# Optimization experiments

Hardware: AMD Instinct MI355X
Metric: run time of the kernel (lower is better)

The kernel has to match this reference:

```python
import jax, jax.numpy as jnp
import numpy as np

B, NB, BS, C, H = 4, 128, 128, 256, 8  # batch, num_blocks, block_size, dim, heads


def setup_inputs() -> dict:
    key = jax.random.key(0)
    ks = jax.random.split(key, 8)
    x = jax.random.normal(ks[0], (B, NB * BS, C), dtype=jnp.float32)
    attn_mask = jax.random.randint(ks[1], (NB, BS, BS + 1), 0, 2, dtype=jnp.int32)
    # guarantee the global-node column is always attendable (avoids all--inf rows)
    attn_mask = attn_mask.at[:, :, BS].set(1)
    edge_feats = jax.random.normal(ks[2], (NB, BS, BS + 1, 4), dtype=jnp.float32)
    w_qkv = jax.random.normal(ks[3], (C, 3 * C), dtype=jnp.float32) * (C ** -0.5)
    b_qkv = jnp.zeros((3 * C,), dtype=jnp.float32)
    w_proj = jax.random.normal(ks[4], (C, C), dtype=jnp.float32) * (C ** -0.5)
    b_proj = jnp.zeros((C,), dtype=jnp.float32)
    w_gate = jax.random.normal(ks[5], (4, H), dtype=jnp.float32) * 0.01  # nn.init.normal_(std=0.01)
    b_gate = jnp.zeros((H,), dtype=jnp.float32)
    return {"x": x, "attn_mask": attn_mask, "edge_feats": edge_feats,
            "w_qkv": w_qkv, "b_qkv": b_qkv, "w_proj": w_proj, "b_proj": b_proj,
            "w_gate": w_gate, "b_gate": b_gate}


def reference(x, attn_mask, edge_feats, w_qkv, b_qkv, w_proj, b_proj, w_gate, b_gate):
    Bv, N, Cv = x.shape
    nb, bs, _ = attn_mask.shape
    Hv = b_gate.shape[0]
    hd = Cv // Hv
    scale = hd ** -0.5

    x_blk = x.reshape(Bv, nb, bs, Cv)
    block_node = x_blk.mean(axis=2, keepdims=True)           # [B, nb, 1, C]
    kv = jnp.concatenate([x_blk, block_node], axis=2)        # [B, nb, bs+1, C]

    qkv_q = x_blk @ w_qkv + b_qkv
    qkv_kv = kv @ w_qkv + b_qkv
    q = qkv_q[..., :Cv].reshape(Bv, nb, bs, Hv, hd)
    k = qkv_kv[..., Cv:2 * Cv].reshape(Bv, nb, bs + 1, Hv, hd)
    v = qkv_kv[..., 2 * Cv:].reshape(Bv, nb, bs + 1, Hv, hd)

    scores = jnp.einsum('bnqhd,bnkhd->bnqkh', q, k) * scale  # [B, nb, bs, bs+1, H]

    # physics bias: zero out (with channel-3 = 1) at the global-node column and the diagonal
    qi = jnp.arange(bs)[:, None]
    ki = jnp.arange(bs + 1)[None, :]
    special = (ki == bs) | (ki == qi)                        # [bs, bs+1]
    special_vec = jnp.array([0.0, 0.0, 0.0, 1.0], dtype=x.dtype)
    bias = jnp.where(special[:, :, None], special_vec, edge_feats[..., :4])  # [nb, bs, bs+1, 4]
    bias = jnp.broadcast_to(bias[None], (Bv, nb, bs, bs + 1, 4))

    scores = scores + bias[..., 3:4]
    mask = (attn_mask[None, :, :, :, None] != 0)             # [1, nb, bs, bs+1, 1]
    scores = jnp.where(mask, scores, -jnp.inf)
    probs = jax.nn.softmax(scores, axis=3)

    gate = jnp.where(mask, bias @ w_gate + b_gate, jnp.zeros((), dtype=x.dtype))
    combined = probs + gate                                  # [B, nb, bs, bs+1, H]

    out = jnp.einsum('bnqkh,bnkhd->bnqhd', combined, v).reshape(Bv, N, Cv)
    return out @ w_proj + b_proj
```

## Files before the change

### kernel.cpp

```cpp
#include <hip/hip_runtime.h>

#define B_   4
#define NB_  128
#define BS_  128
#define C_   256
#define H_   8
#define KL_  129
#define SC2_   0.25503486f
#define LOG2E_ 1.4426950408889634f
#define LN2_   0.6931471805599453f
#define RSTR_  99072

typedef unsigned short u16;
typedef unsigned int   u32;
typedef short          s16;
typedef __attribute__((ext_vector_type(8))) __bf16 bf16x8;
typedef __attribute__((ext_vector_type(4))) float  f32x4;

__device__ __forceinline__ float bf16tof(u16 u) {
  union { u32 i; float f; } v; v.i = ((u32)u) << 16; return v.f;
}
__device__ __forceinline__ u16 fbits(float a) {
  union { __bf16 h; u16 u; } v; v.h = (__bf16)a; return v.u;
}
__device__ __forceinline__ u32 pk2(float a, float b) {
  union { __bf16 h[2]; u32 u; } v;
  v.h[0] = (__bf16)a; v.h[1] = (__bf16)b;
  return v.u;
}
__device__ __forceinline__ float asf(u32 u) {
  union { u32 i; float f; } v; v.i = u; return v.f;
}

__device__ __forceinline__ void glds16(const void* g, void* l) {
  __builtin_amdgcn_global_load_lds(
      (const __attribute__((address_space(1))) unsigned int*)g,
      (__attribute__((address_space(3))) unsigned int*)l, 16, 0, 0);
}

__global__ __launch_bounds__(256) void meancvt_kernel(const float* __restrict__ x,
                                                      u16* __restrict__ xb) {
  const int blk = blockIdx.x;
  const int c = threadIdx.x;
  const float* p = x + (size_t)blk * BS_ * C_ + c;
  u16* q = xb + (size_t)blk * (KL_ * C_) + c;
  float s = 0.f;
  #pragma unroll 4
  for (int r = 0; r < BS_; ++r) {
    const float v = p[(size_t)r * C_];
    s += v;
    q[(size_t)r * C_] = fbits(v);
  }
  q[(size_t)BS_ * C_] = fbits(s * (1.0f / BS_));
}

__global__ __launch_bounds__(256) void wt_kernel(const float* __restrict__ wq,
      const float* __restrict__ wp, s16* __restrict__ wtq, s16* __restrict__ wtp) {
  const int i = blockIdx.x * 256 + threadIdx.x;
  if (i < 768 * 256) {
    const int nn = i >> 8, k = i & 255;
    wtq[i] = (s16)fbits(wq[k * 768 + nn]);
  } else {
    const int j = i - 768 * 256;
    const int nn = j >> 8, k = j & 255;
    wtp[j] = (s16)fbits(wp[k * 256 + nn]);
  }
}

__global__ __launch_bounds__(256) void pre_kernel(const int* __restrict__ mask,
      const float* __restrict__ ef, u16* __restrict__ e4t) {
  const int t = blockIdx.x * 256 + threadIdx.x;
  const int kq = t & 31;
  const int row = t >> 5;
  const int q = row & 127;
  const int key0 = kq * 4;
  const int* mrow = mask + (size_t)row * KL_;
  const float* erow = ef + (size_t)row * KL_ * 4;
  u32 o[8];
  #pragma unroll
  for (int r = 0; r < 4; ++r) {
    const int key = key0 + r;
    const int m = mrow[key];
    float4 e = *(const float4*)(erow + (size_t)key * 4);
    if (key == q) { e.x = 0.f; e.y = 0.f; e.z = 0.f; e.w = 1.f; }
    float e3L = e.w * LOG2E_;
    if (!m) { e.x = 0.f; e.y = 0.f; e.z = 0.f; e3L = -1e30f; }
    o[2*r]   = pk2(e.x, e.y);
    o[2*r+1] = pk2(e.z, e3L);
  }
  uint4* dst = (uint4*)(e4t + (size_t)row * 512 + key0 * 4);
  dst[0] = uint4{o[0], o[1], o[2], o[3]};
  dst[1] = uint4{o[4], o[5], o[6], o[7]};
}

template<bool STRIDED, bool OBF16, int NS>
__global__ __launch_bounds__(256) void mfma_gemm(const s16* __restrict__ Ab,
      const s16* __restrict__ Bt, const float* __restrict__ bias,
      void* __restrict__ outv) {
  __shared__ __align__(16) s16 Al[2][128 * 64];
  __shared__ __align__(16) s16 Bl[2][128 * 64];
  const int tid = threadIdx.x;
  const int lane = tid & 63;
  const int wid = tid >> 6;
  constexpr int ncol = NS / 128;
  const int per  = gridDim.x >> 3;
  const int gidx = (blockIdx.x & 7) * per + (blockIdx.x >> 3);
  const int arow = gidx / ncol;
  const int col0 = (gidx - arow * ncol) * 128;
  const int row0 = arow * 128;
  const int ldrow = lane >> 3;
  const int lcb   = (lane & 7) * 16;

  auto STAGE = [&](int k0, int buf) {
    #pragma unroll
    for (int j = 0; j < 4; ++j) {
      const int c = wid * 4 + j;
      const int row = c * 8 + ldrow;
      const int scb = lcb ^ ((row & 7) << 4);
      glds16(Bt + (size_t)(col0 + row) * C_ + k0 + (scb >> 1), &Bl[buf][c * 512]);
    }
    #pragma unroll
    for (int j = 0; j < 4; ++j) {
      const int c = wid * 4 + j;
      const int row = c * 8 + ldrow;
      const int scb = lcb ^ ((row & 7) << 4);
      if constexpr (STRIDED)
        glds16(Ab + (size_t)arow * RSTR_ + (size_t)row * 768 + 256
                  + k0 + (scb >> 1), &Al[buf][c * 512]);
      else
        glds16(Ab + (size_t)(row0 + row) * C_ + k0 + (scb >> 1), &Al[buf][c * 512]);
    }
  };

  f32x4 acc[4][4];
  #pragma unroll
  for (int i = 0; i < 4; ++i)
    #pragma unroll
    for (int j = 0; j < 4; ++j) acc[i][j] = f32x4{0.f, 0.f, 0.f, 0.f};

  STAGE(0, 0);
  __syncthreads();

  const int fr = lane & 15;
  const int ar0 = (wid >> 1) * 64;
  const int ac0 = (wid & 1) * 64;
  #pragma unroll 1
  for (int t = 0; t < 4; ++t) {
    if (t < 3) STAGE((t + 1) * 64, (t + 1) & 1);
    const char* Ac = (const char*)&Al[t & 1][0];
    const char* Bc = (const char*)&Bl[t & 1][0];
    #pragma unroll
    for (int kk = 0; kk < 64; kk += 32) {
      const int kb = kk * 2 + (lane >> 4) * 16;
      bf16x8 af[4], bfr[4];
      #pragma unroll
      for (int mf = 0; mf < 4; ++mf) {
        const int row = ar0 + mf * 16 + fr;
        af[mf] = *(const bf16x8*)(Ac + row * 128 + (kb ^ ((row & 7) << 4)));
      }
      #pragma unroll
      for (int nf = 0; nf < 4; ++nf) {
        const int row = ac0 + nf * 16 + fr;
        bfr[nf] = *(const bf16x8*)(Bc + row * 128 + (kb ^ ((row & 7) << 4)));
      }
      #pragma unroll
      for (int mf = 0; mf < 4; ++mf)
        #pragma unroll
        for (int nf = 0; nf < 4; ++nf)
          acc[mf][nf] = __builtin_amdgcn_mfma_f32_16x16x32_bf16(
              af[mf], bfr[nf], acc[mf][nf], 0, 0, 0);
    }
    __syncthreads();
  }

  const int orow0 = row0 + (wid >> 1) * 64 + (lane >> 4) * 4;
  const int ocol0 = col0 + (wid & 1) * 64 + (lane & 15);
  #pragma unroll
  for (int nf = 0; nf < 4; ++nf) {
    const int col = ocol0 + nf * 16;
    const float bb = bias[col];
    #pragma unroll
    for (int mf = 0; mf < 4; ++mf) {
      #pragma unroll
      for (int r = 0; r < 4; ++r) {
        const size_t row = (size_t)(orow0 + mf * 16 + r);
        const float v = acc[mf][nf][r] + bb;
        if constexpr (OBF16) ((u16*)outv)[row * NS + col] = fbits(v);
        else                 ((float*)outv)[row * NS + col] = v;
      }
    }
  }
}

__global__ __launch_bounds__(256, 4) void attn_kernel(u16* __restrict__ qkv,
      const u16* __restrict__ e4t, const float* __restrict__ wg_,
      const float* __restrict__ bg) {
  __shared__ __align__(16) char lds[36176];
  const int bid = blockIdx.x;
  const int xcd = bid & 7;
  const int j   = bid >> 3;
  const int wgi = xcd * 64 + (j >> 3);
  const int h   = j & 7;
  const int n = wgi & (NB_ - 1);
  const int tid = threadIdx.x;
  const int wid = tid >> 6, lane = tid & 63;
  const int g = lane >> 4, ql = lane & 15;
  u16*  Kl = (u16*)lds;
  u16*  vt = (u16*)(lds + 10320);
  char* pb = lds + 18768 + wid * 4352;

  u16* qkv_blk = qkv + (size_t)wgi * RSTR_;
  const u16* ebase = e4t + (size_t)n * (128 * 512);

  for (int i = tid; i < 516; i += 256) {
    const int r = i >> 2, dc = i & 3;
    const uint4 u = *(const uint4*)(qkv_blk + (size_t)r * 768 + 256 + h * 32 + dc * 8);
    *(uint4*)(Kl + r * 40 + dc * 8) = u;
  }
  for (int i = tid; i < 512; i += 256) {
    const int r = i >> 2, dc = i & 3;
    const uint4 u = *(const uint4*)(qkv_blk + (size_t)r * 768 + 512 + h * 32 + dc * 8);
    u16* col = vt + (dc * 8) * 132 + r;
    col[0 * 132] = (u16)(u.x & 0xffff); col[1 * 132] = (u16)(u.x >> 16);
    col[2 * 132] = (u16)(u.y & 0xffff); col[3 * 132] = (u16)(u.y >> 16);
    col[4 * 132] = (u16)(u.z & 0xffff); col[5 * 132] = (u16)(u.z >> 16);
    col[6 * 132] = (u16)(u.w & 0xffff); col[7 * 132] = (u16)(u.w >> 16);
  }
  __syncthreads();

  const float v128a = bf16tof(qkv_blk[(size_t)128 * 768 + 512 + h * 32 + ql]);
  const float v128b = bf16tof(qkv_blk[(size_t)128 * 768 + 512 + h * 32 + 16 + ql]);

  const float wgc0 = wg_[h], wgc1 = wg_[8 + h], wgc2 = wg_[16 + h];
  const float wgc3s = wg_[24 + h] * LN2_;
  const float bgh = bg[h];
  const float gk128 = wg_[24 + h] + bgh;

  #pragma unroll 1
  for (int mi = 0; mi < 2; ++mi) {
    const int mt = wid * 2 + mi;
    const int qrow = mt * 16 + ql;
    const bf16x8 qf = *(const bf16x8*)(qkv_blk + (size_t)qrow * 768 + h * 32 + g * 8);
    const uint4* eql = (const uint4*)(ebase + (size_t)qrow * 512) + 2 * g;

    float psum = 0.f;
    uint2 gab[8];
    #pragma unroll
    for (int f = 0; f < 8; ++f) {
      const bf16x8 kf = *(const bf16x8*)(Kl + (16 * f + ql) * 40 + 8 * g);
      f32x4 st = __builtin_amdgcn_mfma_f32_16x16x32_bf16(
          kf, qf, f32x4{0.f, 0.f, 0.f, 0.f}, 0, 0, 0);
      const uint4 ea = eql[8 * f];
      const uint4 eb = eql[8 * f + 1];
      const u32 wa[4] = {ea.x, ea.z, eb.x, eb.z};
      const u32 wb[4] = {ea.y, ea.w, eb.y, eb.w};
      float w[4], gt[4];
      #pragma unroll
      for (int r = 0; r < 4; ++r) {
        const float e0 = asf(wa[r] << 16), e1 = asf(wa[r] & 0xffff0000u);
        const float e2 = asf(wb[r] << 16), e3L = asf(wb[r] & 0xffff0000u);
        const float gg = fmaf(e0, wgc0, fmaf(e1, wgc1,
                          fmaf(e2, wgc2, fmaf(e3L, wgc3s, bgh))));
        gt[r] = (e3L > -1e29f) ? gg : 0.f;
        w[r] = __builtin_amdgcn_exp2f(fmaf(st[r], SC2_, e3L));
        psum += w[r];
      }
      gab[f] = uint2{pk2(gt[0], gt[1]), pk2(gt[2], gt[3])};
      *(uint2*)(pb + ql * 272 + (16 * f + 4 * g) * 2) =
          uint2{pk2(w[0], w[1]), pk2(w[2], w[3])};
    }
    const bf16x8 kf8 = *(const bf16x8*)(Kl + 128 * 40 + 8 * g);
    f32x4 st8 = __builtin_amdgcn_mfma_f32_16x16x32_bf16(
        kf8, qf, f32x4{0.f, 0.f, 0.f, 0.f}, 0, 0, 0);
    const float w0 = __builtin_amdgcn_exp2f(
        fmaf(st8[0], SC2_, (g == 0) ? LOG2E_ : -1e30f));
    psum += w0;
    psum += __shfl_xor(psum, 16);
    psum += __shfl_xor(psum, 32);
    const float inv = __builtin_amdgcn_rcpf(psum);
    const float c128 = fmaf(w0, inv, (g == 0) ? gk128 : 0.f);

    f32x4 ow0{0.f,0.f,0.f,0.f}, ow1{0.f,0.f,0.f,0.f};
    #pragma unroll
    for (int c = 0; c < 4; ++c) {
      const bf16x8 pa = *(const bf16x8*)(pb + ql * 272 + (32 * c + 8 * g) * 2);
      const bf16x8 v0 = *(const bf16x8*)(vt + ql * 132 + 32 * c + 8 * g);
      const bf16x8 v1 = *(const bf16x8*)(vt + (16 + ql) * 132 + 32 * c + 8 * g);
      ow0 = __builtin_amdgcn_mfma_f32_16x16x32_bf16(pa, v0, ow0, 0, 0, 0);
      ow1 = __builtin_amdgcn_mfma_f32_16x16x32_bf16(pa, v1, ow1, 0, 0, 0);
    }
    #pragma unroll
    for (int f = 0; f < 8; ++f)
      *(uint2*)(pb + ql * 272 + (16 * f + 4 * g) * 2) = gab[f];
    f32x4 og0{0.f,0.f,0.f,0.f}, og1{0.f,0.f,0.f,0.f};
    #pragma unroll
    for (int c = 0; c < 4; ++c) {
      const bf16x8 pa = *(const bf16x8*)(pb + ql * 272 + (32 * c + 8 * g) * 2);
      const bf16x8 v0 = *(const bf16x8*)(vt + ql * 132 + 32 * c + 8 * g);
      const bf16x8 v1 = *(const bf16x8*)(vt + (16 + ql) * 132 + 32 * c + 8 * g);
      og0 = __builtin_amdgcn_mfma_f32_16x16x32_bf16(pa, v0, og0, 0, 0, 0);
      og1 = __builtin_amdgcn_mfma_f32_16x16x32_bf16(pa, v1, og1, 0, 0, 0);
    }
    u16* aop = qkv_blk + (size_t)(mt * 16 + g * 4) * 768 + 256 + h * 32 + ql;
    #pragma unroll
    for (int r = 0; r < 4; ++r) {
      const float iv = __shfl(inv,  4 * g + r);
      const float cc = __shfl(c128, 4 * g + r);
      aop[(size_t)r * 768]      = fbits(fmaf(cc, v128a, fmaf(ow0[r], iv, og0[r])));
      aop[(size_t)r * 768 + 16] = fbits(fmaf(cc, v128b, fmaf(ow1[r], iv, og1[r])));
    }
  }
}

extern "C" void kernel_launch(void* const* d_in, const int* in_sizes, int n_in,
                              void* d_out, int out_size, void* d_ws, size_t ws_size,
                              hipStream_t stream) {
  (void)in_sizes; (void)n_in; (void)out_size; (void)ws_size;
  const float* x      = (const float*)d_in[0];
  const int*   mask   = (const int*)  d_in[1];
  const float* ef     = (const float*)d_in[2];
  const float* w_qkv  = (const float*)d_in[3];
  const float* b_qkv  = (const float*)d_in[4];
  const float* w_proj = (const float*)d_in[5];
  const float* b_proj = (const float*)d_in[6];
  const float* w_gate = (const float*)d_in[7];
  const float* b_gate = (const float*)d_in[8];
  float* out = (float*)d_out;
  char* ws = (char*)d_ws;

  u16* qkv = (u16*)(ws);
  s16* wtq = (s16*)(ws + 101449728);
  s16* wtp = (s16*)(ws + 101842944);
  u16* xb  = (u16*)(ws + 101974016);
  u16* e4t = (u16*)(ws + 101974016);

  meancvt_kernel<<<B_ * NB_, 256, 0, stream>>>(x, xb);
  wt_kernel<<<(768 * 256 + 256 * 256) / 256, 256, 0, stream>>>(
      w_qkv, w_proj, wtq, wtp);
  mfma_gemm<false, true, 768>
      <<<(B_ * NB_ * KL_ / 128) * 6, 256, 0, stream>>>(
      (const s16*)xb, wtq, b_qkv, qkv);
  pre_kernel<<<(NB_ * BS_ * 32) / 256, 256, 0, stream>>>(mask, ef, e4t);
  attn_kernel<<<B_ * NB_ * H_, 256, 0, stream>>>(
      qkv, (const u16*)e4t, w_gate, b_gate);
  mfma_gemm<true, false, 256>
      <<<(B_ * NB_ * BS_ / 128) * 2, 256, 0, stream>>>(
      (const s16*)qkv, wtp, b_proj, out);
}
```

Measured before the change: 196.8 us.

## Precompute per-head gate tables and a separate score-bias table in pre_kernel

Result: faster. 190.9 us, median of 2 (-3.0%).

```diff
diff --git a/kernel.cpp b/kernel.cpp
--- a/kernel.cpp
+++ b/kernel.cpp
@@ -8,7 +8,6 @@
 #define KL_  129
 #define SC2_   0.25503486f
 #define LOG2E_ 1.4426950408889634f
-#define LN2_   0.6931471805599453f
 #define RSTR_  99072
 
 typedef unsigned short u16;
@@ -68,29 +67,46 @@
 }
 
 __global__ __launch_bounds__(256) void pre_kernel(const int* __restrict__ mask,
-      const float* __restrict__ ef, u16* __restrict__ e4t) {
+      const float* __restrict__ ef, const float* __restrict__ wg_,
+      const float* __restrict__ bg, u16* __restrict__ g4t,
+      u16* __restrict__ s4t) {
   const int t = blockIdx.x * 256 + threadIdx.x;
   const int kq = t & 31;
   const int row = t >> 5;
+  const int n = row >> 7;
   const int q = row & 127;
   const int key0 = kq * 4;
   const int* mrow = mask + (size_t)row * KL_;
   const float* erow = ef + (size_t)row * KL_ * 4;
-  u32 o[8];
+  float e0[4], e1[4], e2[4], e3[4];
+  int m[4];
   #pragma unroll
   for (int r = 0; r < 4; ++r) {
     const int key = key0 + r;
-    const int m = mrow[key];
-    float4 e = *(const float4*)(erow + (size_t)key * 4);
-    if (key == q) { e.x = 0.f; e.y = 0.f; e.z = 0.f; e.w = 1.f; }
-    float e3L = e.w * LOG2E_;
-    if (!m) { e.x = 0.f; e.y = 0.f; e.z = 0.f; e3L = -1e30f; }
-    o[2*r]   = pk2(e.x, e.y);
-    o[2*r+1] = pk2(e.z, e3L);
-  }
-  uint4* dst = (uint4*)(e4t + (size_t)row * 512 + key0 * 4);
-  dst[0] = uint4{o[0], o[1], o[2], o[3]};
-  dst[1] = uint4{o[4], o[5], o[6], o[7]};
+    m[r] = mrow[key];
+    float4 ev = *(const float4*)(erow + (size_t)key * 4);
+    if (key == q) { ev.x = 0.f; ev.y = 0.f; ev.z = 0.f; ev.w = 1.f; }
+    e0[r] = ev.x; e1[r] = ev.y; e2[r] = ev.z; e3[r] = ev.w;
+  }
+  float s[4];
+  #pragma unroll
+  for (int r = 0; r < 4; ++r) s[r] = m[r] ? e3[r] * LOG2E_ : -1e30f;
+  *(uint2*)(s4t + (size_t)row * 128 + key0) =
+      uint2{pk2(s[0], s[1]), pk2(s[2], s[3])};
+  #pragma unroll
+  for (int h = 0; h < 8; ++h) {
+    const float w0 = wg_[h], w1 = wg_[8 + h], w2 = wg_[16 + h],
+                w3 = wg_[24 + h], bh = bg[h];
+    float gt[4];
+    #pragma unroll
+    for (int r = 0; r < 4; ++r) {
+      const float gg = fmaf(e0[r], w0, fmaf(e1[r], w1,
+                        fmaf(e2[r], w2, fmaf(e3[r], w3, bh))));
+      gt[r] = m[r] ? gg : 0.f;
+    }
+    *(uint2*)(g4t + (((size_t)n * 8 + h) * 128 + q) * 128 + key0) =
+        uint2{pk2(gt[0], gt[1]), pk2(gt[2], gt[3])};
+  }
 }
 
 template<bool STRIDED, bool OBF16, int NS>
@@ -193,8 +209,8 @@
 }
 
 __global__ __launch_bounds__(256, 4) void attn_kernel(u16* __restrict__ qkv,
-      const u16* __restrict__ e4t, const float* __restrict__ wg_,
-      const float* __restrict__ bg) {
+      const u16* __restrict__ g4t, const u16* __restrict__ s4t,
+      const float* __restrict__ wg_, const float* __restrict__ bg) {
   __shared__ __align__(16) char lds[36176];
   const int bid = blockIdx.x;
   const int xcd = bid & 7;
@@ -210,7 +226,8 @@
   char* pb = lds + 18768 + wid * 4352;
 
   u16* qkv_blk = qkv + (size_t)wgi * RSTR_;
-  const u16* ebase = e4t + (size_t)n * (128 * 512);
+  const u16* sbase = s4t + (size_t)n * (128 * 128);
+  const u16* gbase = g4t + ((size_t)n * 8 + h) * (128 * 128);
 
   for (int i = tid; i < 516; i += 256) {
     const int r = i >> 2, dc = i & 3;
@@ -230,18 +247,15 @@
 
   const float v128a = bf16tof(qkv_blk[(size_t)128 * 768 + 512 + h * 32 + ql]);
   const float v128b = bf16tof(qkv_blk[(size_t)128 * 768 + 512 + h * 32 + 16 + ql]);
-
-  const float wgc0 = wg_[h], wgc1 = wg_[8 + h], wgc2 = wg_[16 + h];
-  const float wgc3s = wg_[24 + h] * LN2_;
-  const float bgh = bg[h];
-  const float gk128 = wg_[24 + h] + bgh;
+  const float gk128 = wg_[24 + h] + bg[h];
 
   #pragma unroll 1
   for (int mi = 0; mi < 2; ++mi) {
     const int mt = wid * 2 + mi;
     const int qrow = mt * 16 + ql;
     const bf16x8 qf = *(const bf16x8*)(qkv_blk + (size_t)qrow * 768 + h * 32 + g * 8);
-    const uint4* eql = (const uint4*)(ebase + (size_t)qrow * 512) + 2 * g;
+    const u16* srow = sbase + (size_t)qrow * 128;
+    const u16* grow = gbase + (size_t)qrow * 128;
 
     float psum = 0.f;
     uint2 gab[8];
@@ -250,22 +264,14 @@
       const bf16x8 kf = *(const bf16x8*)(Kl + (16 * f + ql) * 40 + 8 * g);
       f32x4 st = __builtin_amdgcn_mfma_f32_16x16x32_bf16(
           kf, qf, f32x4{0.f, 0.f, 0.f, 0.f}, 0, 0, 0);
-      const uint4 ea = eql[8 * f];
-      const uint4 eb = eql[8 * f + 1];
-      const u32 wa[4] = {ea.x, ea.z, eb.x, eb.z};
-      const u32 wb[4] = {ea.y, ea.w, eb.y, eb.w};
-      float w[4], gt[4];
-      #pragma unroll
-      for (int r = 0; r < 4; ++r) {
-        const float e0 = asf(wa[r] << 16), e1 = asf(wa[r] & 0xffff0000u);
-        const float e2 = asf(wb[r] << 16), e3L = asf(wb[r] & 0xffff0000u);
-        const float gg = fmaf(e0, wgc0, fmaf(e1, wgc1,
-                          fmaf(e2, wgc2, fmaf(e3L, wgc3s, bgh))));
-        gt[r] = (e3L > -1e29f) ? gg : 0.f;
-        w[r] = __builtin_amdgcn_exp2f(fmaf(st[r], SC2_, e3L));
-        psum += w[r];
-      }
-      gab[f] = uint2{pk2(gt[0], gt[1]), pk2(gt[2], gt[3])};
+      const uint2 sv = *(const uint2*)(srow + 16 * f + 4 * g);
+      gab[f] = *(const uint2*)(grow + 16 * f + 4 * g);
+      float w[4];
+      w[0] = __builtin_amdgcn_exp2f(fmaf(st[0], SC2_, asf(sv.x << 16)));
+      w[1] = __builtin_amdgcn_exp2f(fmaf(st[1], SC2_, asf(sv.x & 0xffff0000u)));
+      w[2] = __builtin_amdgcn_exp2f(fmaf(st[2], SC2_, asf(sv.y << 16)));
+      w[3] = __builtin_amdgcn_exp2f(fmaf(st[3], SC2_, asf(sv.y & 0xffff0000u)));
+      psum += (w[0] + w[1]) + (w[2] + w[3]);
       *(uint2*)(pb + ql * 272 + (16 * f + 4 * g) * 2) =
           uint2{pk2(w[0], w[1]), pk2(w[2], w[3])};
     }
@@ -332,7 +338,8 @@
   s16* wtq = (s16*)(ws + 101449728);
   s16* wtp = (s16*)(ws + 101842944);
   u16* xb  = (u16*)(ws + 101974016);
-  u16* e4t = (u16*)(ws + 101974016);
+  u16* g4t = (u16*)(ws + 101974016);
+  u16* s4t = (u16*)d_out;
 
   meancvt_kernel<<<B_ * NB_, 256, 0, stream>>>(x, xb);
   wt_kernel<<<(768 * 256 + 256 * 256) / 256, 256, 0, stream>>>(
@@ -340,9 +347,10 @@
   mfma_gemm<false, true, 768>
       <<<(B_ * NB_ * KL_ / 128) * 6, 256, 0, stream>>>(
       (const s16*)xb, wtq, b_qkv, qkv);
-  pre_kernel<<<(NB_ * BS_ * 32) / 256, 256, 0, stream>>>(mask, ef, e4t);
+  pre_kernel<<<(NB_ * BS_ * 32) / 256, 256, 0, stream>>>(
+      mask, ef, w_gate, b_gate, g4t, s4t);
   attn_kernel<<<B_ * NB_ * H_, 256, 0, stream>>>(
-      qkv, (const u16*)e4t, w_gate, b_gate);
+      qkv, (const u16*)g4t, (const u16*)s4t, w_gate, b_gate);
   mfma_gemm<true, false, 256>
       <<<(B_ * NB_ * BS_ / 128) * 2, 256, 0, stream>>>(
       (const s16*)qkv, wtp, b_proj, out);
```
